# Kernel optimization log

Hardware: AMD Instinct MI355X
Metric: run time of the kernel (lower is better)

## Reference

```python
import jax, jax.numpy as jnp
import numpy as np

T, I, O = 10000, 2048, 512
DT = 0.001
PSP_DECAY = float(np.exp(-DT / 0.02))
OUT_DECAY = float(np.exp(-DT / 0.01))
STDP_C = 1.0
STDP_MU = 0.1
SPIKE_PROB = 0.05


def setup_inputs() -> dict:
    key = jax.random.key(0)
    k1, k2, k3 = jax.random.split(key, 3)
    # Poisson-encoded binary spike trains (as produced by SpikePopulationGroupBatchToTimeEncoder)
    input_spikes = (jax.random.uniform(k1, (T, I)) < SPIKE_PROB).astype(jnp.float32)
    u_rand = jax.random.uniform(k2, (T,), dtype=jnp.float32)  # per-step WTA sampling uniforms
    W = 0.1 * jax.random.normal(k3, (O, I), dtype=jnp.float32)
    b = jnp.zeros((O,), jnp.float32)
    return {"input_spikes": input_spikes, "u_rand": u_rand, "W": W, "b": b}


def _input_psp(spikes):
    # exponential PSP filter along time: psp[t] = decay*psp[t-1] + spikes[t]
    def step(c, s):
        c = PSP_DECAY * c + s
        return c, c
    _, psps = jax.lax.scan(step, jnp.zeros(spikes.shape[1], spikes.dtype), spikes)
    return psps  # [T, I]


def reference(input_spikes, u_rand, W, b):
    psps = _input_psp(input_spikes)
    n_out = W.shape[0]

    def step(carry, inp):
        W, b, trace = carry
        psp, u = inp
        z_in = W @ psp + b                              # linear, [O]
        p = jax.nn.softmax(z_in)                        # stochastic WTA cell
        idx = jnp.minimum(jnp.sum(jnp.cumsum(p) < u), n_out - 1)
        z_out = jax.nn.one_hot(idx, n_out, dtype=psp.dtype)
        trace = OUT_DECAY * trace + z_out               # neuron cell state
        # Bayesian STDP (sequential, depends on previous step's weights)
        dW = z_out[:, None] * (STDP_C * jnp.exp(-W) * psp[None, :] - 1.0)
        db = z_out * (STDP_C * jnp.exp(-b) - 1.0)
        return (W + STDP_MU * dW, b + STDP_MU * db, trace), z_out

    (Wf, bf, trace), z_outs = jax.lax.scan(
        step, (W, b, jnp.zeros_like(b)), (psps, u_rand))
    # matches torch forward's (stacked z_out, final z_state)
    return z_outs, trace
```

## Files before the change

kernel.cpp:

```cpp
#include <hip/hip_runtime.h>
#include <math.h>

static constexpr int T_STEPS = 10000;
static constexpr int I_DIM = 2048;
static constexpr int O_DIM = 512;
static constexpr int NWG = 4;
static constexpr int STRIPE = 128;
static constexpr int WGS = 512;
static constexpr int KPAD = 192;
static constexpr int NSPL = 7;
static constexpr int GN = 19;
static constexpr float PSPD = 0.9512294245007140091f;
static constexpr float OUTD = 0.9048374180359595732f;
static constexpr float MU = 0.1f;

typedef float __attribute__((ext_vector_type(4))) f32x4;
typedef float __attribute__((ext_vector_type(2))) f32x2;

static constexpr size_t WT_BLK = (size_t)(I_DIM + 1) * STRIPE;

__global__ void build_idx_kernel(const float* __restrict__ spikes,
                                 unsigned short* __restrict__ idxl,
                                 int* __restrict__ cnts) {
    int t = blockIdx.x;
    int tid = threadIdx.x;
    if (t >= T_STEPS) {
        for (int p = tid; p < KPAD; p += 256) idxl[(size_t)t * KPAD + p] = (unsigned short)I_DIM;
        if (tid == 0) cnts[t] = 0;
        return;
    }
    const float4* row = reinterpret_cast<const float4*>(spikes + (size_t)t * I_DIM);
    float4 a = row[tid * 2];
    float4 b = row[tid * 2 + 1];
    float v[8] = {a.x, a.y, a.z, a.w, b.x, b.y, b.z, b.w};
    unsigned short tmp[8];
    int c = 0;
#pragma unroll
    for (int j = 0; j < 8; ++j)
        if (v[j] != 0.0f) tmp[c++] = (unsigned short)(tid * 8 + j);

    int lane = tid & 63, wid = tid >> 6;
    int x = c;
    for (int d = 1; d < 64; d <<= 1) {
        int y = __shfl_up(x, d);
        if (lane >= d) x += y;
    }
    __shared__ int wtot[4];
    if (lane == 63) wtot[wid] = x;
    __syncthreads();
    int off = x - c;
    for (int w = 0; w < wid; ++w) off += wtot[w];
    int tot = wtot[0] + wtot[1] + wtot[2] + wtot[3];
    if (tot > KPAD) tot = KPAD;
    for (int j = 0; j < c; ++j) {
        int p = off + j;
        if (p < KPAD) idxl[(size_t)t * KPAD + p] = tmp[j];
    }
    for (int p = tid; p < KPAD; p += 256)
        if (p >= tot) idxl[(size_t)t * KPAD + p] = (unsigned short)I_DIM;
    if (tid == 0) cnts[t] = tot;
}

__global__ void copy_w_kernel(const float* __restrict__ W, float* __restrict__ Wrow) {
    int i = blockIdx.x * blockDim.x + threadIdx.x;
    reinterpret_cast<float4*>(Wrow)[i] = reinterpret_cast<const float4*>(W)[i];
}

__global__ void transpose_kernel(const float* __restrict__ W, float* __restrict__ Wt) {
    __shared__ float tile[32][33];
    int i0 = blockIdx.x * 32;
    int o0 = blockIdx.y * 32;
    int x = threadIdx.x;
    for (int y = threadIdx.y; y < 32; y += 8)
        tile[y][x] = W[(size_t)(o0 + y) * I_DIM + i0 + x];
    __syncthreads();
    for (int y = threadIdx.y; y < 32; y += 8) {
        int o = o0 + x, i = i0 + y;
        Wt[(size_t)(o >> 7) * WT_BLK + (size_t)i * STRIPE + (o & 127)] = tile[x][y];
    }
}

__global__ void zero_pad_row_kernel(float* __restrict__ Wt) {
    int w = threadIdx.x >> 7, c = threadIdx.x & 127;
    Wt[(size_t)w * WT_BLK + (size_t)I_DIM * STRIPE + c] = 0.0f;
}

__device__ __forceinline__ void bar() {
    asm volatile("s_waitcnt lgkmcnt(0)" ::: "memory");
    __builtin_amdgcn_sched_barrier(0);
    __builtin_amdgcn_s_barrier();
    __builtin_amdgcn_sched_barrier(0);
}

__device__ __forceinline__ float wave_max_dpp(float x) {
    int xb = __float_as_int(x);
#define DPPSTEPM(ctrl, rm)                                                          \
    {                                                                               \
        int tt = __builtin_amdgcn_update_dpp(0xff800000, xb, ctrl, rm, 0xf, false); \
        xb = __float_as_int(fmaxf(__int_as_float(xb), __int_as_float(tt)));         \
    }
    DPPSTEPM(0x111, 0xf)
    DPPSTEPM(0x112, 0xf)
    DPPSTEPM(0x114, 0xf)
    DPPSTEPM(0x118, 0xf)
    DPPSTEPM(0x142, 0xa)
    DPPSTEPM(0x143, 0xc)
#undef DPPSTEPM
    return __int_as_float(__builtin_amdgcn_readlane(xb, 63));
}

__device__ __forceinline__ float dpp_scan_add(float x) {
#define DPPSTEPA(ctrl, rm)                                                          \
    {                                                                               \
        float tt = __int_as_float(                                                  \
            __builtin_amdgcn_update_dpp(0, __float_as_int(x), ctrl, rm, 0xf, false)); \
        x += tt;                                                                    \
    }
    DPPSTEPA(0x111, 0xf)
    DPPSTEPA(0x112, 0xf)
    DPPSTEPA(0x114, 0xf)
    DPPSTEPA(0x118, 0xf)
    DPPSTEPA(0x142, 0xa)
    DPPSTEPA(0x143, 0xc)
#undef DPPSTEPA
    return x;
}

__launch_bounds__(WGS, 1)
__global__ void seq_kernel(const unsigned short* __restrict__ idxl,
                           const int* __restrict__ cnts,
                           const float* __restrict__ u_rand,
                           const float* __restrict__ b_in,
                           float* __restrict__ Wrow,
                           float* __restrict__ Wt,
                           unsigned long long* __restrict__ slots,
                           float* __restrict__ out) {
    __shared__ __align__(16) float psp[I_DIM + 4];
    __shared__ __align__(16) float mk0[I_DIM + 4];
    __shared__ __align__(16) float mk1[I_DIM + 4];
    __shared__ f32x2 sg[2][NSPL][64];
    __shared__ float redE[8], redF[8], redG[2][8];
    __shared__ unsigned short sidx[3][KPAD];
    __shared__ int s_rr, s_own;

    const int w = blockIdx.x;
    const int tid = threadIdx.x;
    const int lane = tid & 63;
    const int jw = tid >> 6;
    const int i4 = tid * 4;
    const int o0 = w * STRIPE;
    float* __restrict__ WtS = Wt + (size_t)w * WT_BLK;
    const unsigned long long wt_base = (unsigned long long)WtS;

    for (int p = tid; p < I_DIM + 4; p += WGS) { psp[p] = 0.0f; mk0[p] = 0.0f; mk1[p] = 0.0f; }
    for (int p = tid; p < 3 * KPAD; p += WGS) ((unsigned short*)sidx)[p] = idxl[p];
    if (tid == 0) { s_rr = 0; s_own = 0; }
    __syncthreads();
    const int cnt0 = cnts[0];
    if (tid < KPAD) {
        psp[sidx[0][tid]] = 1.0f;
        mk1[sidx[1][tid]] = 1.0f;
    }
    __syncthreads();
    if (jw > 0) {
        float a0 = 0.0f, a1 = 0.0f;
        for (int k = jw - 1; k < cnt0; k += NSPL) {
            int col = sidx[0][k];
            f32x2 v = *(const f32x2*)(WtS + (size_t)col * STRIPE + lane * 2);
            a0 += v.x; a1 += v.y;
        }
        sg[0][jw - 1][lane] = (f32x2){a0, a1};
    }
    float aA0 = 0.0f, aA1 = 0.0f, b0 = 0.0f, b1 = 0.0f, tr0 = 0.0f, tr1 = 0.0f;
    if (jw == 0) { b0 = b_in[o0 + 2 * lane]; b1 = b_in[o0 + 2 * lane + 1]; }
    int own1 = 0, own2 = 0, col1 = 0, col2 = 0;
    float nw0 = 0.0f, nw1 = 0.0f, nw2 = 0.0f, nw3 = 0.0f;
    int cnt_use = cnts[1];
    float u_cur = u_rand[0];
    __syncthreads();

    for (int t = 0; t < T_STEPS; ++t) {
        const int par = t & 1;
        const int cb = par;
        const int nb = par ^ 1;
        float* mcur = par ? mk1 : mk0;
        float* mnxt = par ? mk0 : mk1;

        float u_nxt; int cnt_fut;
        {
            const float* up = u_rand + (t + 1 < T_STEPS ? t + 1 : T_STEPS - 1);
            asm volatile("global_load_dword %0, %1, off" : "=&v"(u_nxt) : "v"(up) : "memory");
            const int* cp = cnts + (t + 2);
            asm volatile("global_load_dword %0, %1, off" : "=&v"(cnt_fut) : "v"(cp) : "memory");
        }
        unsigned int pfw = 0;
        if (tid >= 256 && tid < 256 + KPAD / 2) {
            const unsigned int* pp = reinterpret_cast<const unsigned int*>(idxl) +
                                     (size_t)(t + 3) * (KPAD / 2) + (tid - 256);
            asm volatile("global_load_dword %0, %1, off" : "=&v"(pfw) : "v"(pp) : "memory");
        }
        f32x4 mreg = (f32x4){0.0f, 0.0f, 0.0f, 0.0f};
        f32x4 pr = (f32x4){0.0f, 0.0f, 0.0f, 0.0f};

        if (jw > 0) {
            f32x2 vals[GN];
            {
                const unsigned short* lst = sidx[(t + 1) % 3];
                const int kw = jw - 1;
#pragma unroll
                for (int j = 0; j < GN; ++j) {
                    int col = lst[kw + NSPL * j];
                    unsigned int voff = ((unsigned)col << 9) | ((unsigned)lane << 3);
                    asm volatile("global_load_dwordx2 %0, %1, %2"
                                 : "=&v"(vals[j]) : "v"(voff), "s"(wt_base) : "memory");
                }
            }
            mreg = *(const f32x4*)(mnxt + i4);
            if (own1) {
                float gp2 = nw0 * mreg.x + nw1 * mreg.y + nw2 * mreg.z + nw3 * mreg.w;
                float gs = dpp_scan_add(gp2);
                if (lane == 63) redG[par][jw] = gs;
            }
            *(f32x4*)(mcur + i4) = (f32x4){0.0f, 0.0f, 0.0f, 0.0f};
            pr = *(const f32x4*)(psp + i4);
            {
#pragma clang fp contract(off)
                float q0 = pr.x * PSPD; q0 += mreg.x;
                float q1 = pr.y * PSPD; q1 += mreg.y;
                float q2 = pr.z * PSPD; q2 += mreg.z;
                float q3 = pr.w * PSPD; q3 += mreg.w;
                *(f32x4*)(psp + i4) = (f32x4){q0, q1, q2, q3};
            }
            asm volatile("s_waitcnt vmcnt(0)" ::: "memory");
            __builtin_amdgcn_sched_barrier(0);
            asm volatile("" : "+v"(cnt_fut), "+v"(u_nxt));
            {
                float a0 = vals[0].x, a1 = vals[0].y;
#pragma unroll
                for (int j = 1; j < GN; ++j) { a0 += vals[j].x; a1 += vals[j].y; }
                if (cnt_use > NSPL * GN) {
                    const unsigned short* lst = sidx[(t + 1) % 3];
                    for (int k = NSPL * GN + (jw - 1); k < cnt_use; k += NSPL) {
                        int col = lst[k];
                        f32x2 v = *(const f32x2*)(WtS + (size_t)col * STRIPE + lane * 2);
                        a0 += v.x; a1 += v.y;
                    }
                }
                sg[nb][jw - 1][lane] = (f32x2){a0, a1};
            }
            if (tid >= 256 && tid < 256 + KPAD / 2)
                ((unsigned int*)sidx[(t + 3) % 3])[tid - 256] = pfw;
        } else {
            tr0 *= OUTD; tr1 *= OUTD;
            float v0 = 0.0f, v1 = 0.0f;
#pragma unroll
            for (int j = 0; j < NSPL; ++j) { f32x2 s = sg[cb][j][lane]; v0 += s.x; v1 += s.y; }
            if (own1) {
                float es = 0.0f, fs = 0.0f;
#pragma unroll
                for (int j = 0; j < 8; ++j) { es += redE[j]; fs += redF[j]; }
                if (lane == (col1 >> 1)) {
                    if (col1 & 1) { aA1 += es; v1 = fs; } else { aA0 += es; v0 = fs; }
                }
            }
            if (own2 && !(own1 && col2 == col1)) {
                float gs = 0.0f;
#pragma unroll
                for (int j = 0; j < 8; ++j) gs += redG[par ^ 1][j];
                if (lane == (col2 >> 1)) { if (col2 & 1) v1 = gs; else v0 = gs; }
            }
            aA0 = PSPD * aA0 + v0; aA1 = PSPD * aA1 + v1;
            float z0 = aA0 + b0, z1 = aA1 + b1;
            float m_w = wave_max_dpp(fmaxf(z0, z1));
            float e0 = expf(z0 - m_w), e1 = expf(z1 - m_w);
            float pin = dpp_scan_add(e0 + e1);
            float pex = __int_as_float(
                __builtin_amdgcn_update_dpp(0, __float_as_int(pin), 0x111, 0xf, 0xf, false));
            float p15 = __int_as_float(__builtin_amdgcn_readlane(__float_as_int(pin), 15));
            float p31 = __int_as_float(__builtin_amdgcn_readlane(__float_as_int(pin), 31));
            float p47 = __int_as_float(__builtin_amdgcn_readlane(__float_as_int(pin), 47));
            if (lane == 16) pex = p15;
            if (lane == 32) pex = p31;
            if (lane == 48) pex = p47;
            float S_w = __int_as_float(__builtin_amdgcn_readlane(__float_as_int(pin), 63));
            unsigned long long tag = ((unsigned long long)(unsigned)(t + 1)) << 32;
            if (lane == 0) {
                unsigned long long* my = slots + (((size_t)par * NWG + w) * 2);
                __hip_atomic_store(my + 0, tag | (unsigned)__float_as_int(m_w),
                                   __ATOMIC_RELAXED, __HIP_MEMORY_SCOPE_AGENT);
                __hip_atomic_store(my + 1, tag | (unsigned)__float_as_int(S_w),
                                   __ATOMIC_RELAXED, __HIP_MEMORY_SCOPE_AGENT);
            }
            int oi = lane >> 1; oi += (oi >= w) ? 1 : 0; oi &= 3;
            unsigned long long* sp = slots + (((size_t)par * NWG + oi) * 2 + (lane & 1));
            bool need = (lane < 6);
            unsigned long long want = (unsigned long long)(unsigned)(t + 1);
            unsigned long long got = 0;
            bool ok = !need;
            int it = 0;
            while (!__all(ok)) {
                if (!ok) {
                    got = __hip_atomic_load(sp, __ATOMIC_RELAXED, __HIP_MEMORY_SCOPE_AGENT);
                    ok = ((got >> 32) == want);
                }
                if (++it > (1 << 22)) break;
            }
            float pay = __int_as_float((int)(unsigned)got);
            float mj[4], sj[4];
#pragma unroll
            for (int j = 0; j < 4; ++j) {
                if (j == w) { mj[j] = m_w; sj[j] = S_w; }
                else {
                    int pos = j - (j > w ? 1 : 0);
                    mj[j] = __shfl(pay, 2 * pos);
                    sj[j] = __shfl(pay, 2 * pos + 1);
                }
            }
            float M = fmaxf(fmaxf(mj[0], mj[1]), fmaxf(mj[2], mj[3]));
            float o_run = 0.0f, offw = 0.0f, offn = 0.0f, sc_w = 0.0f;
#pragma unroll
            for (int j = 0; j < 4; ++j) {
                float sc = expf(mj[j] - M);
                if (j == w) { offw = o_run; sc_w = sc; }
                o_run = fmaf(sj[j], sc, o_run);
                if (j == w) offn = o_run;
            }
            float uQ = u_cur * o_run;
            int owner = (((offw < uQ) || w == 0) && ((uQ <= offn) || w == NWG - 1)) ? 1 : 0;
            if (lane == 0) { s_own = owner; s_rr = STRIPE - 1; }
            if (owner) {
                float cqp0 = fmaf(pex, sc_w, offw);
                float cq0  = fmaf(pex + e0, sc_w, offw);
                float cq1  = fmaf(pin, sc_w, offw);
                bool firstG = (w == 0 && lane == 0);
                bool lastG  = (w == NWG - 1 && lane == 63);
                bool w0c = (cqp0 < uQ || firstG) && (uQ <= cq0);
                bool w1c = (cq0 < uQ) && (uQ <= cq1 || lastG);
                if (w0c) s_rr = 2 * lane;
                if (w1c) s_rr = 2 * lane + 1;
            }
            asm volatile("s_waitcnt vmcnt(0)" ::: "memory");
            __builtin_amdgcn_sched_barrier(0);
            asm volatile("" : "+v"(cnt_fut), "+v"(u_nxt));
            mreg = *(const f32x4*)(mnxt + i4);
            if (own1) {
                float gp2 = nw0 * mreg.x + nw1 * mreg.y + nw2 * mreg.z + nw3 * mreg.w;
                float gs = dpp_scan_add(gp2);
                if (lane == 63) redG[par][0] = gs;
            }
            *(f32x4*)(mcur + i4) = (f32x4){0.0f, 0.0f, 0.0f, 0.0f};
            pr = *(const f32x4*)(psp + i4);
            {
#pragma clang fp contract(off)
                float q0 = pr.x * PSPD; q0 += mreg.x;
                float q1 = pr.y * PSPD; q1 += mreg.y;
                float q2 = pr.z * PSPD; q2 += mreg.z;
                float q3 = pr.w * PSPD; q3 += mreg.w;
                *(f32x4*)(psp + i4) = (f32x4){q0, q1, q2, q3};
            }
        }
        bar();

        const int rr = s_rr;
        const int own = s_own;
        const int rrglob = o0 + rr;
        f32x4 w2 = (f32x4){0.0f, 0.0f, 0.0f, 0.0f};
        if (own) {
            const float* rp = Wrow + (size_t)rrglob * I_DIM + i4;
            asm volatile("global_load_dwordx4 %0, %1, off" : "=&v"(w2) : "v"(rp) : "memory");
        }
        if (tid < KPAD) mcur[sidx[(t + 2) % 3][tid]] = 1.0f;
        if (own) {
            asm volatile("s_waitcnt vmcnt(0)" ::: "memory");
            __builtin_amdgcn_sched_barrier(0);
            nw0 = w2.x + MU * (expf(-w2.x) * pr.x - 1.0f);
            nw1 = w2.y + MU * (expf(-w2.y) * pr.y - 1.0f);
            nw2 = w2.z + MU * (expf(-w2.z) * pr.z - 1.0f);
            nw3 = w2.w + MU * (expf(-w2.w) * pr.w - 1.0f);
            *(f32x4*)(Wrow + (size_t)rrglob * I_DIM + i4) = (f32x4){nw0, nw1, nw2, nw3};
            WtS[(size_t)(i4 + 0) * STRIPE + rr] = nw0;
            WtS[(size_t)(i4 + 1) * STRIPE + rr] = nw1;
            WtS[(size_t)(i4 + 2) * STRIPE + rr] = nw2;
            WtS[(size_t)(i4 + 3) * STRIPE + rr] = nw3;
            float dp = (nw0 - w2.x) * pr.x + (nw1 - w2.y) * pr.y +
                       (nw2 - w2.z) * pr.z + (nw3 - w2.w) * pr.w;
            float gp = nw0 * mreg.x + nw1 * mreg.y + nw2 * mreg.z + nw3 * mreg.w;
            float ds = dpp_scan_add(dp);
            float gs = dpp_scan_add(gp);
            if (lane == 63) { redE[jw] = ds; redF[jw] = gs; }
            if (jw == 0 && lane == (rr >> 1)) {
                if (rr & 1) { tr1 += 1.0f; b1 = b1 + MU * (expf(-b1) - 1.0f); }
                else        { tr0 += 1.0f; b0 = b0 + MU * (expf(-b0) - 1.0f); }
                out[(size_t)t * O_DIM + rrglob] = 1.0f;
            }
        }
        own2 = own1; col2 = col1;
        own1 = own;  col1 = rr;
        cnt_use = cnt_fut;
        u_cur = u_nxt;
        bar();
    }

    if (jw == 0) {
        out[(size_t)T_STEPS * O_DIM + o0 + 2 * lane] = tr0;
        out[(size_t)T_STEPS * O_DIM + o0 + 2 * lane + 1] = tr1;
    }
}

extern "C" void kernel_launch(void* const* d_in, const int* in_sizes, int n_in,
                              void* d_out, int out_size, void* d_ws, size_t ws_size,
                              hipStream_t stream) {
    const float* spikes = (const float*)d_in[0];
    const float* u_rand = (const float*)d_in[1];
    const float* W      = (const float*)d_in[2];
    const float* b      = (const float*)d_in[3];
    float* out = (float*)d_out;

    float* Wrow = (float*)d_ws;
    float* Wt   = Wrow + (size_t)O_DIM * I_DIM;
    unsigned short* idxl = (unsigned short*)(Wt + (size_t)NWG * WT_BLK);
    int* cnts = (int*)(idxl + (size_t)(T_STEPS + 4) * KPAD);
    unsigned long long* slots = (unsigned long long*)(cnts + (T_STEPS + 4));

    hipMemsetAsync(d_out, 0, (size_t)out_size * sizeof(float), stream);
    hipMemsetAsync(slots, 0, 2 * NWG * 2 * sizeof(unsigned long long), stream);

    hipLaunchKernelGGL(build_idx_kernel, dim3(T_STEPS + 4), dim3(256), 0, stream,
                       spikes, idxl, cnts);
    hipLaunchKernelGGL(copy_w_kernel, dim3((O_DIM * I_DIM / 4) / 256), dim3(256), 0, stream,
                       W, Wrow);
    hipLaunchKernelGGL(transpose_kernel, dim3(I_DIM / 32, O_DIM / 32), dim3(32, 8), 0, stream,
                       W, Wt);
    hipLaunchKernelGGL(zero_pad_row_kernel, dim3(1), dim3(NWG * STRIPE), 0, stream, Wt);
    hipLaunchKernelGGL(seq_kernel, dim3(NWG), dim3(WGS), 0, stream,
                       idxl, cnts, u_rand, b, Wrow, Wt, slots, out);
}
```

Baseline: 27.75 ms.

## Co-locate sequential workgroups on one XCC and poll via device atomics

Launches 32 workgroups. Each one reads its XCC id and claims a slot through a per-XCC counter, and the first XCC to gather four workgroups wins the roles while the others exit. The cross-workgroup softmax max/sum exchange now polls with atomic OR read-modify-writes on a separate cache-line-padded buffer, with a plain atomic load as a fallback every eighth iteration. The intent is to keep the per-step inter-workgroup handshake inside one XCC's L2 and lower its latency. The cost is extra launch and role-election work, plus reliance on undocumented XCC placement and on atomics being served at L2.

Result: slower. 30.29 ms (+9.1%).

```diff
diff --git a/kernel.cpp b/kernel.cpp
--- a/kernel.cpp
+++ b/kernel.cpp
@@ -5,6 +5,7 @@
 static constexpr int I_DIM = 2048;
 static constexpr int O_DIM = 512;
 static constexpr int NWG = 4;
+static constexpr int NLAUNCH = 32;
 static constexpr int STRIPE = 128;
 static constexpr int WGS = 512;
 static constexpr int KPAD = 192;
@@ -133,7 +134,9 @@
                            const float* __restrict__ b_in,
                            float* __restrict__ Wrow,
                            float* __restrict__ Wt,
-                           unsigned long long* __restrict__ slots,
+                           unsigned long long* __restrict__ slow,
+                           unsigned long long* __restrict__ fastp,
+                           int* __restrict__ ctrl,
                            float* __restrict__ out) {
     __shared__ __align__(16) float psp[I_DIM + 4];
     __shared__ __align__(16) float mk0[I_DIM + 4];
@@ -141,12 +144,38 @@
     __shared__ f32x2 sg[2][NSPL][64];
     __shared__ float redE[8], redF[8], redG[2][8];
     __shared__ unsigned short sidx[3][KPAD];
-    __shared__ int s_rr, s_own;
-
-    const int w = blockIdx.x;
+    __shared__ int s_rr, s_own, s_role;
+
     const int tid = threadIdx.x;
     const int lane = tid & 63;
     const int jw = tid >> 6;
+
+    if (tid == 0) {
+        unsigned xcc;
+        asm volatile("s_getreg_b32 %0, hwreg(HW_REG_XCC_ID)" : "=s"(xcc));
+        xcc &= 7;
+        int pos = __hip_atomic_fetch_add(&ctrl[xcc], 1, __ATOMIC_RELAXED,
+                                         __HIP_MEMORY_SCOPE_AGENT);
+        int role = -1;
+        if (pos < NWG) {
+            if (pos == NWG - 1) {
+                int expected = 0;
+                __hip_atomic_compare_exchange_strong(&ctrl[8], &expected, (int)xcc + 1,
+                                                     __ATOMIC_RELAXED, __ATOMIC_RELAXED,
+                                                     __HIP_MEMORY_SCOPE_AGENT);
+            }
+            int L = 0, itc = 0;
+            do {
+                L = __hip_atomic_load(&ctrl[8], __ATOMIC_RELAXED, __HIP_MEMORY_SCOPE_AGENT);
+            } while (L == 0 && ++itc < (1 << 24));
+            if (L == (int)xcc + 1) role = pos;
+        }
+        s_role = role;
+    }
+    __syncthreads();
+    const int w = s_role;
+    if (w < 0) return;
+
     const int i4 = tid * 4;
     const int o0 = w * STRIPE;
     float* __restrict__ WtS = Wt + (size_t)w * WT_BLK;
@@ -284,24 +313,36 @@
             if (lane == 48) pex = p47;
             float S_w = __int_as_float(__builtin_amdgcn_readlane(__float_as_int(pin), 63));
             unsigned long long tag = ((unsigned long long)(unsigned)(t + 1)) << 32;
+            unsigned long long pm = tag | (unsigned)__float_as_int(m_w);
+            unsigned long long ps = tag | (unsigned)__float_as_int(S_w);
             if (lane == 0) {
-                unsigned long long* my = slots + (((size_t)par * NWG + w) * 2);
-                __hip_atomic_store(my + 0, tag | (unsigned)__float_as_int(m_w),
-                                   __ATOMIC_RELAXED, __HIP_MEMORY_SCOPE_AGENT);
-                __hip_atomic_store(my + 1, tag | (unsigned)__float_as_int(S_w),
-                                   __ATOMIC_RELAXED, __HIP_MEMORY_SCOPE_AGENT);
+                unsigned long long* fl = fastp + ((size_t)par * NWG + w) * 8;
+                asm volatile("global_atomic_swap_x2 %0, %1, off" :: "v"(fl), "v"(pm) : "memory");
+                asm volatile("global_atomic_swap_x2 %0, %1, off" :: "v"(fl + 1), "v"(ps) : "memory");
+                unsigned long long* my = slow + (((size_t)par * NWG + w) * 2);
+                __hip_atomic_store(my + 0, pm, __ATOMIC_RELAXED, __HIP_MEMORY_SCOPE_AGENT);
+                __hip_atomic_store(my + 1, ps, __ATOMIC_RELAXED, __HIP_MEMORY_SCOPE_AGENT);
             }
             int oi = lane >> 1; oi += (oi >= w) ? 1 : 0; oi &= 3;
-            unsigned long long* sp = slots + (((size_t)par * NWG + oi) * 2 + (lane & 1));
+            unsigned long long* sp = slow + (((size_t)par * NWG + oi) * 2 + (lane & 1));
+            unsigned long long* fp = fastp + ((size_t)par * NWG + oi) * 8 + (lane & 1);
             bool need = (lane < 6);
-            unsigned long long want = (unsigned long long)(unsigned)(t + 1);
             unsigned long long got = 0;
             bool ok = !need;
             int it = 0;
             while (!__all(ok)) {
                 if (!ok) {
-                    got = __hip_atomic_load(sp, __ATOMIC_RELAXED, __HIP_MEMORY_SCOPE_AGENT);
-                    ok = ((got >> 32) == want);
+                    unsigned long long g;
+                    if ((it & 7) == 7) {
+                        g = __hip_atomic_load(sp, __ATOMIC_RELAXED, __HIP_MEMORY_SCOPE_AGENT);
+                    } else {
+                        unsigned long long z64 = 0;
+                        asm volatile("global_atomic_or_x2 %0, %1, %2, off sc0"
+                                     : "=&v"(g) : "v"(fp), "v"(z64) : "memory");
+                        asm volatile("s_waitcnt vmcnt(0)" ::: "memory");
+                        __builtin_amdgcn_sched_barrier(0);
+                    }
+                    if ((g >> 32) == (unsigned long long)(unsigned)(t + 1)) { got = g; ok = true; }
                 }
                 if (++it > (1 << 22)) break;
             }
@@ -420,10 +461,13 @@
     float* Wt   = Wrow + (size_t)O_DIM * I_DIM;
     unsigned short* idxl = (unsigned short*)(Wt + (size_t)NWG * WT_BLK);
     int* cnts = (int*)(idxl + (size_t)(T_STEPS + 4) * KPAD);
-    unsigned long long* slots = (unsigned long long*)(cnts + (T_STEPS + 4));
+    unsigned long long* slow = (unsigned long long*)(cnts + (T_STEPS + 4));
+    unsigned long long* fastp = (unsigned long long*)
+        ((((size_t)(slow + 16)) + 63) & ~(size_t)63);
+    int* ctrl = (int*)(fastp + 2 * NWG * 8);
 
     hipMemsetAsync(d_out, 0, (size_t)out_size * sizeof(float), stream);
-    hipMemsetAsync(slots, 0, 2 * NWG * 2 * sizeof(unsigned long long), stream);
+    hipMemsetAsync(slow, 0, (size_t)((char*)(ctrl + 16) - (char*)slow), stream);
 
     hipLaunchKernelGGL(build_idx_kernel, dim3(T_STEPS + 4), dim3(256), 0, stream,
                        spikes, idxl, cnts);
@@ -432,6 +476,6 @@
     hipLaunchKernelGGL(transpose_kernel, dim3(I_DIM / 32, O_DIM / 32), dim3(32, 8), 0, stream,
                        W, Wt);
     hipLaunchKernelGGL(zero_pad_row_kernel, dim3(1), dim3(NWG * STRIPE), 0, stream, Wt);
-    hipLaunchKernelGGL(seq_kernel, dim3(NWG), dim3(WGS), 0, stream,
-                       idxl, cnts, u_rand, b, Wrow, Wt, slots, out);
-}
+    hipLaunchKernelGGL(seq_kernel, dim3(NLAUNCH), dim3(WGS), 0, stream,
+                       idxl, cnts, u_rand, b, Wrow, Wt, slow, fastp, ctrl, out);
+}
```
